# Kernel optimization log

Hardware: AMD Instinct MI355X
Metric: run time of the kernel (lower is better)

The kernel has to match this reference:

```python
import jax, jax.numpy as jnp
import numpy as np

BLANK = 0


def setup_inputs() -> dict:
    key = jax.random.key(0)
    k1, k2 = jax.random.split(key)
    B, T, V = 64, 4096, 128
    feature = jax.random.normal(k1, (B, T, V), dtype=jnp.float32)
    lengths = jax.random.randint(k2, (B,), 1, T + 1, dtype=jnp.int32)
    return {"feature": feature, "lengths": lengths, "beam_width": 1}


def reference(feature, lengths, beam_width):
    # Greedy CTC decode (beam_width <= 1 path of the torch module), fully vectorized.
    # feature: (B, T, V) raw logits; lengths: (B,) valid frame counts.
    B, T, V = feature.shape
    logp = jax.nn.log_softmax(feature.astype(jnp.float32), axis=-1)  # (B, T, V)
    max_scores = jnp.max(logp, axis=-1)                               # (B, T)
    tokens = jnp.argmax(logp, axis=-1).astype(jnp.int32)              # (B, T)

    tmask = jnp.arange(T)[None, :] < lengths[:, None]                 # (B, T) valid frames
    logp_scores = jnp.sum(jnp.where(tmask, max_scores, 0.0), axis=-1) # (B,)

    # CTC collapse: keep token iff it is not blank and differs from previous frame's token.
    # (t != prev or prev == blank) and t != blank  ==  (t != blank) and (t != prev)
    prev = jnp.concatenate(
        [jnp.full((B, 1), BLANK, dtype=tokens.dtype), tokens[:, :-1]], axis=1
    )
    keep = (tokens != BLANK) & (tokens != prev) & tmask               # (B, T)

    # Fixed-shape encoding of the ragged prediction lists:
    # tokens[b, t] is part of prediction[b] (in time order) wherever keep[b, t].
    return tokens, keep, logp_scores
```

## Files before the change

### kernel.cpp

```cpp
#include <hip/hip_runtime.h>

#define BLANK 0

__global__ __launch_bounds__(256) void ctc_rowmax(const float* __restrict__ feat,
                                                  const int* __restrict__ lengths,
                                                  float* __restrict__ out_tok,
                                                  float* __restrict__ partial,
                                                  int npairs, int Tshift, int Tmask)
{
    const int lane = threadIdx.x & 63;
    const int l32  = lane & 31;
    const int half = lane >> 5;
    const int wid  = (blockIdx.x * 256 + (int)threadIdx.x) >> 6;
    const int nw   = (gridDim.x * 256) >> 6;
    const int nquads = npairs >> 2;

    for (int q = wid; q < nquads; q += nw) {
        const int pair0 = q << 2;
        const float4* base = (const float4*)feat + (size_t)pair0 * 64;
        float4 v0 = base[lane];
        float4 v1 = base[64 + lane];
        float4 v2 = base[128 + lane];
        float4 v3 = base[192 + lane];

        const int row0 = pair0 << 1;
        const int len  = lengths[row0 >> Tshift];
        float acc = 0.0f;

        auto process = [&](float4 v, int pair) {
            float m = v.x; int li = 0;
            if (v.y > m) { m = v.y; li = 1; }
            if (v.z > m) { m = v.z; li = 2; }
            if (v.w > m) { m = v.w; li = 3; }
            const float lm  = m;
            const int  lidx = (l32 << 2) + li;
            float s = __expf(v.x) + __expf(v.y) + __expf(v.z) + __expf(v.w);
            #pragma unroll
            for (int off = 16; off >= 1; off >>= 1) {
                m  = fmaxf(m, __shfl_xor(m, off, 64));
                s += __shfl_xor(s, off, 64);
            }
            unsigned long long bal = __ballot(lm == m);
            unsigned seg = half ? (unsigned)(bal >> 32) : (unsigned)bal;
            int src = (__ffs(seg) - 1) | (half << 5);
            int idx = __shfl(lidx, src, 64);
            const int row = (pair << 1) + half;
            if (l32 == 0) {
                out_tok[row] = (float)idx;
                if ((row & Tmask) < len) acc += m - __logf(s);
            }
        };
        process(v0, pair0);
        process(v1, pair0 + 1);
        process(v2, pair0 + 2);
        process(v3, pair0 + 3);

        acc += __shfl_xor(acc, 32, 64);
        if (lane == 0) partial[row0 >> 3] = acc;
    }
}

__global__ __launch_bounds__(256) void ctc_collapse(const int* __restrict__ lengths,
                                                    const float* __restrict__ out_tok,
                                                    const float* __restrict__ partial,
                                                    float* __restrict__ keep,
                                                    float* __restrict__ scores,
                                                    int T, int Tdiv8)
{
    const int b = blockIdx.y;
    const int t = blockIdx.x * 256 + (int)threadIdx.x;
    const size_t base = (size_t)b * T;
    if (t < T) {
        float tk = out_tok[base + t];
        float pv = (t == 0) ? (float)BLANK : out_tok[base + t - 1];
        bool valid = t < lengths[b];
        keep[base + t] = (tk != (float)BLANK && tk != pv && valid) ? 1.0f : 0.0f;
    }
    if (blockIdx.x == 0) {
        float s = 0.0f;
        for (int i = threadIdx.x; i < Tdiv8; i += 256)
            s += partial[(size_t)b * Tdiv8 + i];
        #pragma unroll
        for (int off = 32; off >= 1; off >>= 1) s += __shfl_xor(s, off, 64);
        __shared__ float red[4];
        if ((threadIdx.x & 63) == 0) red[threadIdx.x >> 6] = s;
        __syncthreads();
        if (threadIdx.x == 0) scores[b] = red[0] + red[1] + red[2] + red[3];
    }
}

extern "C" void kernel_launch(void* const* d_in, const int* in_sizes, int n_in,
                              void* d_out, int out_size, void* d_ws, size_t ws_size,
                              hipStream_t stream) {
    const float* feat    = (const float*)d_in[0];
    const int*   lengths = (const int*)d_in[1];

    const int V  = 128;
    const int B  = in_sizes[1];
    const int T  = in_sizes[0] / (B * V);
    const int BT = B * T;

    float* out_tok = (float*)d_out;
    float* keep    = out_tok + (size_t)BT;
    float* scores  = out_tok + (size_t)2 * BT;
    float* partial = (float*)d_ws;

    int Tshift = 31 - __builtin_clz((unsigned)T);
    int Tmask  = T - 1;
    int npairs = BT >> 1;

    ctc_rowmax<<<2048, 256, 0, stream>>>(feat, lengths, out_tok, partial,
                                         npairs, Tshift, Tmask);

    dim3 g2((T + 255) / 256, B);
    ctc_collapse<<<g2, 256, 0, stream>>>(lengths, out_tok, partial, keep, scores,
                                         T, T >> 3);
}
```

Measured before the change: 191.8 us.

## Fuse CTC collapse into rowmax pass with 32-row spans per wave

Each wavefront now handles a 32-row span, with sixteen float4 loads issued up front instead of a grid-stride loop over four loads. Tokens are gathered into lanes so the keep mask is computed in registers and written in the first pass. The second kernel only fixes the span-boundary keep entries and reduces the per-span score partials, one block per batch row. This removes the full re-read of tokens and the separate keep pass, at the cost of more register pressure from sixteen float4 values per thread and a grid sized to the data.

Result: slower. 200.6 us (+4.6%).

```diff
diff --git a/kernel.cpp b/kernel.cpp
--- a/kernel.cpp
+++ b/kernel.cpp
@@ -2,91 +2,94 @@
 
 #define BLANK 0
 
-__global__ __launch_bounds__(256) void ctc_rowmax(const float* __restrict__ feat,
-                                                  const int* __restrict__ lengths,
-                                                  float* __restrict__ out_tok,
-                                                  float* __restrict__ partial,
-                                                  int npairs, int Tshift, int Tmask)
+__global__ __launch_bounds__(256) void ctc_pass1(const float* __restrict__ feat,
+                                                 const int* __restrict__ lengths,
+                                                 float* __restrict__ out_tok,
+                                                 float* __restrict__ keep,
+                                                 float* __restrict__ partial,
+                                                 int nspans, int Tshift, int Tmask)
 {
     const int lane = threadIdx.x & 63;
     const int l32  = lane & 31;
     const int half = lane >> 5;
-    const int wid  = (blockIdx.x * 256 + (int)threadIdx.x) >> 6;
-    const int nw   = (gridDim.x * 256) >> 6;
-    const int nquads = npairs >> 2;
+    const int w    = (blockIdx.x * 256 + (int)threadIdx.x) >> 6;
+    if (w >= nspans) return;
 
-    for (int q = wid; q < nquads; q += nw) {
-        const int pair0 = q << 2;
-        const float4* base = (const float4*)feat + (size_t)pair0 * 64;
-        float4 v0 = base[lane];
-        float4 v1 = base[64 + lane];
-        float4 v2 = base[128 + lane];
-        float4 v3 = base[192 + lane];
+    const float4* base = (const float4*)feat + (size_t)w * 1024;
+    float4 v[16];
+    #pragma unroll
+    for (int j = 0; j < 16; ++j) v[j] = base[(j << 6) + lane];
 
-        const int row0 = pair0 << 1;
-        const int len  = lengths[row0 >> Tshift];
-        float acc = 0.0f;
+    const int row0 = w << 5;
+    const int t0   = row0 & Tmask;
+    const int len  = lengths[row0 >> Tshift];
 
-        auto process = [&](float4 v, int pair) {
-            float m = v.x; int li = 0;
-            if (v.y > m) { m = v.y; li = 1; }
-            if (v.z > m) { m = v.z; li = 2; }
-            if (v.w > m) { m = v.w; li = 3; }
-            const float lm  = m;
-            const int  lidx = (l32 << 2) + li;
-            float s = __expf(v.x) + __expf(v.y) + __expf(v.z) + __expf(v.w);
-            #pragma unroll
-            for (int off = 16; off >= 1; off >>= 1) {
-                m  = fmaxf(m, __shfl_xor(m, off, 64));
-                s += __shfl_xor(s, off, 64);
-            }
-            unsigned long long bal = __ballot(lm == m);
-            unsigned seg = half ? (unsigned)(bal >> 32) : (unsigned)bal;
-            int src = (__ffs(seg) - 1) | (half << 5);
-            int idx = __shfl(lidx, src, 64);
-            const int row = (pair << 1) + half;
-            if (l32 == 0) {
-                out_tok[row] = (float)idx;
-                if ((row & Tmask) < len) acc += m - __logf(s);
-            }
-        };
-        process(v0, pair0);
-        process(v1, pair0 + 1);
-        process(v2, pair0 + 2);
-        process(v3, pair0 + 3);
+    float acc  = 0.0f;
+    float tokf = 0.0f;
 
-        acc += __shfl_xor(acc, 32, 64);
-        if (lane == 0) partial[row0 >> 3] = acc;
+    #pragma unroll
+    for (int j = 0; j < 16; ++j) {
+        const float4 vv = v[j];
+        float m = vv.x; int li = 0;
+        if (vv.y > m) { m = vv.y; li = 1; }
+        if (vv.z > m) { m = vv.z; li = 2; }
+        if (vv.w > m) { m = vv.w; li = 3; }
+        const float lm  = m;
+        const int  lidx = (l32 << 2) + li;
+        float s = __expf(vv.x) + __expf(vv.y) + __expf(vv.z) + __expf(vv.w);
+        #pragma unroll
+        for (int off = 16; off >= 1; off >>= 1) {
+            m  = fmaxf(m, __shfl_xor(m, off, 64));
+            s += __shfl_xor(s, off, 64);
+        }
+        unsigned long long bal = __ballot(lm == m);
+        unsigned seg = half ? (unsigned)(bal >> 32) : (unsigned)bal;
+        int src = (__ffs(seg) - 1) | (half << 5);
+        int idx = __shfl(lidx, src, 64);
+        int idxo = __shfl(idx, lane | 32, 64);
+        if (lane == 2 * j)     tokf = (float)idx;
+        if (lane == 2 * j + 1) tokf = (float)idxo;
+        if (l32 == 0 && (t0 + 2 * j + half) < len) acc += m - __logf(s);
     }
+
+    float pv = __shfl(tokf, lane - 1, 64);
+    bool valid = (t0 + lane) < len;
+    float kp = (tokf != (float)BLANK && tokf != pv && valid) ? 1.0f : 0.0f;
+    if (lane < 32) {
+        out_tok[row0 + lane] = tokf;
+        if (lane >= 1) keep[row0 + lane] = kp;
+    }
+
+    acc += __shfl_xor(acc, 32, 64);
+    if (lane == 0) partial[w] = acc;
 }
 
-__global__ __launch_bounds__(256) void ctc_collapse(const int* __restrict__ lengths,
-                                                    const float* __restrict__ out_tok,
-                                                    const float* __restrict__ partial,
-                                                    float* __restrict__ keep,
-                                                    float* __restrict__ scores,
-                                                    int T, int Tdiv8)
+__global__ __launch_bounds__(128) void ctc_pass2(const int* __restrict__ lengths,
+                                                 const float* __restrict__ out_tok,
+                                                 const float* __restrict__ partial,
+                                                 float* __restrict__ keep,
+                                                 float* __restrict__ scores,
+                                                 int T)
 {
-    const int b = blockIdx.y;
-    const int t = blockIdx.x * 256 + (int)threadIdx.x;
+    const int b   = blockIdx.x;
+    const int nsp = T >> 5;
     const size_t base = (size_t)b * T;
-    if (t < T) {
+    const int len = lengths[b];
+
+    float s = 0.0f;
+    for (int i = threadIdx.x; i < nsp; i += blockDim.x) {
+        s += partial[(size_t)b * nsp + i];
+        const int t = i << 5;
         float tk = out_tok[base + t];
         float pv = (t == 0) ? (float)BLANK : out_tok[base + t - 1];
-        bool valid = t < lengths[b];
-        keep[base + t] = (tk != (float)BLANK && tk != pv && valid) ? 1.0f : 0.0f;
+        keep[base + t] = (tk != (float)BLANK && tk != pv && t < len) ? 1.0f : 0.0f;
     }
-    if (blockIdx.x == 0) {
-        float s = 0.0f;
-        for (int i = threadIdx.x; i < Tdiv8; i += 256)
-            s += partial[(size_t)b * Tdiv8 + i];
-        #pragma unroll
-        for (int off = 32; off >= 1; off >>= 1) s += __shfl_xor(s, off, 64);
-        __shared__ float red[4];
-        if ((threadIdx.x & 63) == 0) red[threadIdx.x >> 6] = s;
-        __syncthreads();
-        if (threadIdx.x == 0) scores[b] = red[0] + red[1] + red[2] + red[3];
-    }
+    #pragma unroll
+    for (int off = 32; off >= 1; off >>= 1) s += __shfl_xor(s, off, 64);
+    __shared__ float red[2];
+    if ((threadIdx.x & 63) == 0) red[threadIdx.x >> 6] = s;
+    __syncthreads();
+    if (threadIdx.x == 0) scores[b] = red[0] + red[1];
 }
 
 extern "C" void kernel_launch(void* const* d_in, const int* in_sizes, int n_in,
@@ -107,12 +110,10 @@
 
     int Tshift = 31 - __builtin_clz((unsigned)T);
     int Tmask  = T - 1;
-    int npairs = BT >> 1;
+    int nspans = BT >> 5;
 
-    ctc_rowmax<<<2048, 256, 0, stream>>>(feat, lengths, out_tok, partial,
-                                         npairs, Tshift, Tmask);
+    ctc_pass1<<<(nspans + 3) / 4, 256, 0, stream>>>(feat, lengths, out_tok, keep,
+                                                    partial, nspans, Tshift, Tmask);
 
-    dim3 g2((T + 255) / 256, B);
-    ctc_collapse<<<g2, 256, 0, stream>>>(lengths, out_tok, partial, keep, scores,
-                                         T, T >> 3);
+    ctc_pass2<<<B, 128, 0, stream>>>(lengths, out_tok, partial, keep, scores, T);
 }
```
